# Kernel tuning notes

Measured on AMD Instinct MI355X. Metric: run time of the kernel, lower is better.

Reference implementation:

```python
import jax, jax.numpy as jnp
import numpy as np

HIDDEN = 1024
N_HEAD = 16
LN_EPS = 1e-5


def _layernorm(x, g, b):
    m = jnp.mean(x, axis=-1, keepdims=True)
    v = jnp.var(x, axis=-1, keepdims=True)
    return (x - m) * jax.lax.rsqrt(v + LN_EPS) * g + b


def setup_inputs() -> dict:
    key = jax.random.key(0)
    ks = jax.random.split(key, 16)
    H = HIDDEN
    s = 0.02
    d = dict(
        x=jax.random.normal(ks[0], (4, 1024, H), jnp.float32),
        Wq=jax.random.normal(ks[1], (H, H), jnp.float32) * s,
        bq=jnp.zeros((H,), jnp.float32),
        Wk=jax.random.normal(ks[2], (H, H), jnp.float32) * s,
        bk=jnp.zeros((H,), jnp.float32),
        Wv=jax.random.normal(ks[3], (H, H), jnp.float32) * s,
        bv=jnp.zeros((H,), jnp.float32),
        Wo=jax.random.normal(ks[4], (H, H), jnp.float32) * s,
        bo=jnp.zeros((H,), jnp.float32),
        g1=jax.random.normal(ks[5], (H,), jnp.float32) * s,
        b1=jnp.zeros((H,), jnp.float32),
        W1=jax.random.normal(ks[6], (H, 4 * H), jnp.float32) * s,
        c1=jnp.zeros((4 * H,), jnp.float32),
        W2=jax.random.normal(ks[7], (4 * H, H), jnp.float32) * s,
        c2=jnp.zeros((H,), jnp.float32),
        g2=jax.random.normal(ks[8], (H,), jnp.float32) * s,
        b2=jnp.zeros((H,), jnp.float32),
    )
    return d


def reference(x, Wq, bq, Wk, bk, Wv, bv, Wo, bo, g1, b1, W1, c1, W2, c2, g2, b2):
    N, T, Hd = x.shape
    Hh = N_HEAD
    D = Hd // Hh
    # faithful to torch code: .view(N, H, T, D) is a raw reshape, no transpose
    q = (x @ Wq + bq).reshape(N, Hh, T, D)
    k = (x @ Wk + bk).reshape(N, Hh, T, D)
    v = (x @ Wv + bv).reshape(N, Hh, T, D)
    scores = jnp.einsum('nhtd,nhsd->nhts', q, k) / jnp.sqrt(jnp.float32(Hd))
    # faithful: softmax over dim=1 (the head axis)
    attn = jax.nn.softmax(scores, axis=1)
    o = jnp.einsum('nhts,nhsd->nhtd', attn, v).reshape(N, T, Hd)
    o = o @ Wo + bo
    x1 = _layernorm(o + x, g1, b1)
    ff = jax.nn.gelu(x1 @ W1 + c1, approximate=False) @ W2 + c2
    return _layernorm(ff + x1, g2, b2)
```

## Files before the change

### kernel.cpp

```cpp
#include <hip/hip_runtime.h>
#include <cstdint>
#include <cstddef>

#define EPI_QKV  0
#define EPI_F32  2
#define EPI_GELU 3
#define EPI_PART 4

typedef __attribute__((ext_vector_type(8))) short bfrag8;
typedef __attribute__((ext_vector_type(4))) float facc4;

struct PtrQuad { unsigned short* p[4]; };

__device__ __forceinline__ unsigned short f2b(float x) {
  unsigned int u = __builtin_bit_cast(unsigned int, x);
  u += 0x7FFFu + ((u >> 16) & 1u);
  return (unsigned short)(u >> 16);
}
__device__ __forceinline__ float b2f(unsigned short u) {
  unsigned int x = ((unsigned int)u) << 16;
  return __builtin_bit_cast(float, x);
}

__device__ __forceinline__ void gl2lds16(const unsigned short* g, unsigned short* l) {
  __builtin_amdgcn_global_load_lds(
      (const __attribute__((address_space(1))) unsigned int*)g,
      (__attribute__((address_space(3))) unsigned int*)l, 16, 0, 0);
}

__global__ __launch_bounds__(256)
void cvt_bf16_kernel(const float* __restrict__ in, unsigned short* __restrict__ out, int n4) {
  const int i = blockIdx.x * 256 + threadIdx.x;
  if (i < n4) {
    const float4 v = ((const float4*)in)[i];
    ushort4 u;
    u.x = f2b(v.x); u.y = f2b(v.y); u.z = f2b(v.z); u.w = f2b(v.w);
    ((ushort4*)out)[i] = u;
  }
}

__global__ __launch_bounds__(256)
void transpose_cvt(const float* __restrict__ in, unsigned short* __restrict__ out,
                   int K, int N) {
  __shared__ float tile[32][33];
  const int n0 = blockIdx.x * 32;
  const int k0 = blockIdx.y * 32;
  const int tx = threadIdx.x & 31, ty = threadIdx.x >> 5;
#pragma unroll
  for (int i = 0; i < 32; i += 8)
    tile[ty + i][tx] = in[(size_t)(k0 + ty + i) * N + n0 + tx];
  __syncthreads();
#pragma unroll
  for (int i = 0; i < 32; i += 8)
    out[(size_t)(n0 + ty + i) * K + k0 + tx] = f2b(tile[tx][ty + i]);
}

template<int EPI>
__global__ __launch_bounds__(256, 2)
void gemm_bt(const unsigned short* __restrict__ A,
             const unsigned short* __restrict__ Bt,
             const float* __restrict__ bias,
             const float* __restrict__ bias2,
             const float* __restrict__ bias3,
             void* __restrict__ out, PtrQuad pq,
             int M, int N, int K, int ldk) {
  __shared__ unsigned short sA[128 * 32];
  __shared__ unsigned short sB[128 * 32];
  const int tid  = threadIdx.x;
  const int lane = tid & 63;
  const int wave = tid >> 6;
  const int l15  = lane & 15, l4 = lane >> 4;
  const int wr = wave >> 1, wc = wave & 1;
  const long row0 = (long)blockIdx.y * 128;
  const long col0 = (long)blockIdx.x * 128;
  const long k0   = (long)blockIdx.z * K;

  facc4 acc[4][4];
#pragma unroll
  for (int i = 0; i < 4; i++)
#pragma unroll
    for (int j = 0; j < 4; j++) acc[i][j] = (facc4)0.f;

  const int srow = tid >> 2;
  const int scol = (tid & 3) * 8;
  const unsigned short* Ap0 = A  + (row0 + srow) * (long)ldk + k0 + scol;
  const unsigned short* Ap1 = Ap0 + 64 * (long)ldk;
  const unsigned short* Bp0 = Bt + (col0 + srow) * (long)ldk + k0 + scol;
  const unsigned short* Bp1 = Bp0 + 64 * (long)ldk;
  const int wbase = (tid & ~63) * 8;
  unsigned short* sA0 = &sA[wbase];
  unsigned short* sA1 = &sA[2048 + wbase];
  unsigned short* sB0 = &sB[wbase];
  unsigned short* sB1 = &sB[2048 + wbase];

  const int aoff = (wr * 64 + l15) * 32 + l4 * 8;
  const int boff = (wc * 64 + l15) * 32 + l4 * 8;

  for (int kt = 0; kt < K; kt += 32) {
    gl2lds16(Ap0 + kt, sA0);
    gl2lds16(Ap1 + kt, sA1);
    gl2lds16(Bp0 + kt, sB0);
    gl2lds16(Bp1 + kt, sB1);
    __syncthreads();
    bfrag8 af[4], bf[4];
#pragma unroll
    for (int i = 0; i < 4; i++) af[i] = *(const bfrag8*)&sA[aoff + i * 512];
#pragma unroll
    for (int j = 0; j < 4; j++) bf[j] = *(const bfrag8*)&sB[boff + j * 512];
#pragma unroll
    for (int i = 0; i < 4; i++)
#pragma unroll
      for (int j = 0; j < 4; j++)
        acc[i][j] = __builtin_amdgcn_mfma_f32_16x16x32_bf16(af[i], bf[j], acc[i][j], 0, 0, 0);
    __syncthreads();
  }

#pragma unroll
  for (int i = 0; i < 4; i++) {
    const long m0 = row0 + wr * 64 + i * 16 + l4 * 4;
#pragma unroll
    for (int j = 0; j < 4; j++) {
      const long c = col0 + wc * 64 + j * 16 + l15;
      if constexpr (EPI == EPI_QKV) {
        const long which = c >> 10;
        const long cl = c & 1023;
        unsigned short* oq = (unsigned short*)out;
        if (which == 0) {
          const float bj = bias[cl];
#pragma unroll
          for (int r = 0; r < 4; r++)
            oq[(m0 + r) * 1024 + cl] = f2b((acc[i][j][r] + bj) * 0.03125f);
        } else if (which == 1) {
          const float bj = bias2[cl];
#pragma unroll
          for (int r = 0; r < 4; r++)
            (oq + 4194304)[(m0 + r) * 1024 + cl] = f2b(acc[i][j][r] + bj);
        } else {
          const float bj = bias3[cl];
          const long cc = cl >> 6, d = cl & 63;
#pragma unroll
          for (int r = 0; r < 4; r++) {
            const long m = m0 + r;
            const long nbb = m >> 10, rr = m & 1023;
            const long h = rr >> 6, rhi = rr & 63;
            const long s = rhi * 16 + cc;
            (oq + 8388608)[((nbb * 16 + h) * 64 + d) * 1024 + s] = f2b(acc[i][j][r] + bj);
          }
        }
      } else if constexpr (EPI == EPI_F32) {
        const float bj = bias[c];
        float* of = (float*)out;
#pragma unroll
        for (int r = 0; r < 4; r++) of[(m0 + r) * (long)N + c] = acc[i][j][r] + bj;
      } else if constexpr (EPI == EPI_PART) {
        unsigned short* ob = pq.p[blockIdx.z];
#pragma unroll
        for (int r = 0; r < 4; r++) ob[(m0 + r) * (long)N + c] = f2b(acc[i][j][r]);
      } else {
        const float bj = bias[c];
        unsigned short* ob = (unsigned short*)out;
#pragma unroll
        for (int r = 0; r < 4; r++) {
          const float t = acc[i][j][r] + bj;
          ob[(m0 + r) * (long)N + c] = f2b(0.5f * t * (1.f + erff(t * 0.70710678f)));
        }
      }
    }
  }
}

__global__ __launch_bounds__(512, 4)
void attn_kernel(const unsigned short* __restrict__ Qb,
                 const unsigned short* __restrict__ Kb,
                 const unsigned short* __restrict__ Vt,
                 unsigned short* __restrict__ P0, unsigned short* __restrict__ P1) {
  const int id = blockIdx.x;
  const int combo = id & 7;
  const int tile = id >> 3;
  const int nb = combo & 3;
  const int sp = combo >> 2;
  const int tid = threadIdx.x, lane = tid & 63;
  const int w = __builtin_amdgcn_readfirstlane(tid >> 6);
  const int l15 = lane & 15, l4 = lane >> 4;
  const int t0 = tile * 16;

  __shared__ float red[2][8][576];
  __shared__ __align__(16) unsigned short abuf[8][16][40];

  const size_t hb0 = (size_t)(nb * 16 + w * 2) << 16;
  const unsigned short* qB = Qb + hb0;
  const unsigned short* kB = Kb + hb0;
  const unsigned short* vB = Vt + hb0;

  bfrag8 qf[2][2];
#pragma unroll
  for (int hh = 0; hh < 2; hh++)
#pragma unroll
    for (int ks = 0; ks < 2; ks++)
      qf[hh][ks] = *(const bfrag8*)(qB + (hh << 16) + (t0 + l15) * 64 + ks * 32 + l4 * 8);

  facc4 oacc[2][4];
#pragma unroll
  for (int hh = 0; hh < 2; hh++)
#pragma unroll
    for (int nt = 0; nt < 4; nt++) oacc[hh][nt] = (facc4)0.f;

  for (int it = 0; it < 16; ++it) {
    const int s0 = sp * 512 + it * 32;
    const int pb = it & 1;
    facc4 sacc[2][2];
#pragma unroll
    for (int hh = 0; hh < 2; hh++)
#pragma unroll
      for (int nt = 0; nt < 2; nt++) sacc[hh][nt] = (facc4)0.f;
#pragma unroll
    for (int hh = 0; hh < 2; hh++) {
      const unsigned short* kh = kB + (hh << 16);
#pragma unroll
      for (int ks = 0; ks < 2; ks++)
#pragma unroll
        for (int nt = 0; nt < 2; nt++) {
          const bfrag8 kf = *(const bfrag8*)(kh + (s0 + nt * 16 + l15) * 64 + ks * 32 + l4 * 8);
          sacc[hh][nt] = __builtin_amdgcn_mfma_f32_16x16x32_bf16(qf[hh][ks], kf, sacc[hh][nt], 0, 0, 0);
        }
    }
    bfrag8 vf0[4], vf1[4];
#pragma unroll
    for (int nt = 0; nt < 4; nt++) {
      vf0[nt] = *(const bfrag8*)(vB + (size_t)(nt * 16 + l15) * 1024 + s0 + l4 * 8);
      vf1[nt] = *(const bfrag8*)(vB + (1 << 16) + (size_t)(nt * 16 + l15) * 1024 + s0 + l4 * 8);
    }
#pragma unroll
    for (int nt = 0; nt < 2; nt++)
#pragma unroll
      for (int r = 0; r < 4; r++) {
        const float e0 = __expf(sacc[0][nt][r]);
        const float e1 = __expf(sacc[1][nt][r]);
        sacc[0][nt][r] = e0; sacc[1][nt][r] = e1;
        red[pb][w][(l4 * 4 + r) * 36 + nt * 16 + l15] = e0 + e1;
      }
    __syncthreads();
    float rinv[2][4];
#pragma unroll
    for (int nt = 0; nt < 2; nt++)
#pragma unroll
      for (int r = 0; r < 4; r++) {
        const int o = (l4 * 4 + r) * 36 + nt * 16 + l15;
        float s = 0.f;
#pragma unroll
        for (int ww = 0; ww < 8; ww++) s += red[pb][ww][o];
        rinv[nt][r] = 1.f / s;
      }
#pragma unroll
    for (int nt = 0; nt < 2; nt++)
#pragma unroll
      for (int r = 0; r < 4; r++)
        abuf[w][l4 * 4 + r][nt * 16 + l15] = f2b(sacc[0][nt][r] * rinv[nt][r]);
    {
      const bfrag8 af0 = *(const bfrag8*)&abuf[w][l15][l4 * 8];
#pragma unroll
      for (int nt = 0; nt < 4; nt++)
        oacc[0][nt] = __builtin_amdgcn_mfma_f32_16x16x32_bf16(af0, vf0[nt], oacc[0][nt], 0, 0, 0);
    }
#pragma unroll
    for (int nt = 0; nt < 2; nt++)
#pragma unroll
      for (int r = 0; r < 4; r++)
        abuf[w][l4 * 4 + r][nt * 16 + l15] = f2b(sacc[1][nt][r] * rinv[nt][r]);
    {
      const bfrag8 af1 = *(const bfrag8*)&abuf[w][l15][l4 * 8];
#pragma unroll
      for (int nt = 0; nt < 4; nt++)
        oacc[1][nt] = __builtin_amdgcn_mfma_f32_16x16x32_bf16(af1, vf1[nt], oacc[1][nt], 0, 0, 0);
    }
  }
  unsigned short* P = sp ? P1 : P0;
#pragma unroll
  for (int hh = 0; hh < 2; hh++) {
    const size_t rb = ((size_t)nb * 1024 + (size_t)(w * 2 + hh) * 64 + tile) * 1024;
#pragma unroll
    for (int nt = 0; nt < 4; nt++)
#pragma unroll
      for (int r = 0; r < 4; r++)
        P[rb + (size_t)(l4 * 4 + r) * 64 + nt * 16 + l15] = f2b(oacc[hh][nt][r]);
  }
}

__global__ __launch_bounds__(256)
void reduce_o2(const unsigned short* __restrict__ P0, const unsigned short* __restrict__ P1,
               unsigned short* __restrict__ OB, int n4) {
  const int i = blockIdx.x * 256 + threadIdx.x;
  if (i < n4) {
    const ushort4 a = ((const ushort4*)P0)[i];
    const ushort4 b = ((const ushort4*)P1)[i];
    ushort4 u;
    u.x = f2b(b2f(a.x) + b2f(b.x));
    u.y = f2b(b2f(a.y) + b2f(b.y));
    u.z = f2b(b2f(a.z) + b2f(b.z));
    u.w = f2b(b2f(a.w) + b2f(b.w));
    ((ushort4*)OB)[i] = u;
  }
}

__global__ __launch_bounds__(256)
void ln_red(const unsigned short* __restrict__ P0, const unsigned short* __restrict__ P1,
            const unsigned short* __restrict__ P2, const unsigned short* __restrict__ P3,
            const float* __restrict__ bias, const float* __restrict__ resid,
            const float* __restrict__ g, const float* __restrict__ be,
            float* __restrict__ outf, unsigned short* __restrict__ outb) {
  const int row = blockIdx.x, tid = threadIdx.x;
  const size_t o4 = (size_t)row * 256 + tid;
  const ushort4 a = ((const ushort4*)P0)[o4];
  const ushort4 b = ((const ushort4*)P1)[o4];
  const ushort4 c = ((const ushort4*)P2)[o4];
  const ushort4 d = ((const ushort4*)P3)[o4];
  const float4 vb = ((const float4*)bias)[tid];
  const float4 vr = ((const float4*)resid)[o4];
  float t0 = b2f(a.x) + b2f(b.x) + b2f(c.x) + b2f(d.x) + vb.x + vr.x;
  float t1 = b2f(a.y) + b2f(b.y) + b2f(c.y) + b2f(d.y) + vb.y + vr.y;
  float t2 = b2f(a.z) + b2f(b.z) + b2f(c.z) + b2f(d.z) + vb.z + vr.z;
  float t3 = b2f(a.w) + b2f(b.w) + b2f(c.w) + b2f(d.w) + vb.w + vr.w;
  float s = t0 + t1 + t2 + t3;
  float q = t0 * t0 + t1 * t1 + t2 * t2 + t3 * t3;
#pragma unroll
  for (int off = 32; off > 0; off >>= 1) {
    s += __shfl_down(s, off, 64);
    q += __shfl_down(q, off, 64);
  }
  __shared__ float rs_[4], rq_[4];
  if ((tid & 63) == 0) { rs_[tid >> 6] = s; rq_[tid >> 6] = q; }
  __syncthreads();
  const float S = rs_[0] + rs_[1] + rs_[2] + rs_[3];
  const float Q = rq_[0] + rq_[1] + rq_[2] + rq_[3];
  const float mean = S * (1.f / 1024.f);
  const float var  = Q * (1.f / 1024.f) - mean * mean;
  const float rstd = rsqrtf(var + 1e-5f);
  const float4 vg  = ((const float4*)g)[tid];
  const float4 vbe = ((const float4*)be)[tid];
  float o0 = (t0 - mean) * rstd * vg.x + vbe.x;
  float o1 = (t1 - mean) * rstd * vg.y + vbe.y;
  float o2 = (t2 - mean) * rstd * vg.z + vbe.z;
  float o3 = (t3 - mean) * rstd * vg.w + vbe.w;
  ((float4*)(outf + (size_t)row * 1024))[tid] = make_float4(o0, o1, o2, o3);
  if (outb != nullptr) {
    ushort4 u;
    u.x = f2b(o0); u.y = f2b(o1); u.z = f2b(o2); u.w = f2b(o3);
    ((ushort4*)(outb + (size_t)row * 1024))[tid] = u;
  }
}

extern "C" void kernel_launch(void* const* d_in, const int* in_sizes, int n_in,
                              void* d_out, int out_size, void* d_ws, size_t ws_size,
                              hipStream_t stream) {
  const float* x  = (const float*)d_in[0];
  const float* Wq = (const float*)d_in[1];
  const float* bq = (const float*)d_in[2];
  const float* Wk = (const float*)d_in[3];
  const float* bk = (const float*)d_in[4];
  const float* Wv = (const float*)d_in[5];
  const float* bv = (const float*)d_in[6];
  const float* Wo = (const float*)d_in[7];
  const float* bo = (const float*)d_in[8];
  const float* g1 = (const float*)d_in[9];
  const float* b1 = (const float*)d_in[10];
  const float* W1 = (const float*)d_in[11];
  const float* c1 = (const float*)d_in[12];
  const float* W2 = (const float*)d_in[13];
  const float* c2 = (const float*)d_in[14];
  const float* g2 = (const float*)d_in[15];
  const float* b2 = (const float*)d_in[16];
  float* out = (float*)d_out;

  char* ws = (char*)d_ws;
  unsigned short* XB  = (unsigned short*)(ws);
  unsigned short* WQT = (unsigned short*)(ws + 8388608);
  unsigned short* WKT = (unsigned short*)(ws + 10485760);
  unsigned short* WVT = (unsigned short*)(ws + 12582912);
  unsigned short* WOT = (unsigned short*)(ws + 14680064);
  unsigned short* W1T = (unsigned short*)(ws + 16777216);
  unsigned short* W2T = (unsigned short*)(ws + 25165824);
  float*          X1  = (float*)(ws + 33554432);
  unsigned short* X1B = (unsigned short*)(ws + 50331648);
  char* RB = ws + 58720256;
  unsigned short* QB  = (unsigned short*)(RB);
  unsigned short* KB  = (unsigned short*)(RB + 8388608);
  unsigned short* VT  = (unsigned short*)(RB + 16777216);
  unsigned short* OB  = (unsigned short*)(RB + 25165824);
  unsigned short* H1B = (unsigned short*)(RB);
  unsigned short* AP0 = (unsigned short*)(RB + 33554432);
  unsigned short* AP1 = (unsigned short*)(RB + 41943040);
  PtrQuad OPQ = { { QB, KB, VT, XB } };
  PtrQuad FPQ = { { XB, X1B, (unsigned short*)(RB + 33554432),
                    (unsigned short*)(RB + 41943040) } };
  PtrQuad ZQ = { { nullptr, nullptr, nullptr, nullptr } };

  const dim3 tb(256);
  cvt_bf16_kernel<<<dim3(4096), tb, 0, stream>>>(x, XB, 1048576);
  transpose_cvt<<<dim3(32, 32),  tb, 0, stream>>>(Wq, WQT, 1024, 1024);
  transpose_cvt<<<dim3(32, 32),  tb, 0, stream>>>(Wk, WKT, 1024, 1024);
  transpose_cvt<<<dim3(32, 32),  tb, 0, stream>>>(Wv, WVT, 1024, 1024);
  transpose_cvt<<<dim3(32, 32),  tb, 0, stream>>>(Wo, WOT, 1024, 1024);
  transpose_cvt<<<dim3(128, 32), tb, 0, stream>>>(W1, W1T, 1024, 4096);
  transpose_cvt<<<dim3(32, 128), tb, 0, stream>>>(W2, W2T, 4096, 1024);
  gemm_bt<EPI_QKV><<<dim3(24, 32), tb, 0, stream>>>(XB, WQT, bq, bk, bv, (void*)QB, ZQ,
                                                    4096, 3072, 1024, 1024);
  attn_kernel<<<dim3(512), dim3(512), 0, stream>>>(QB, KB, VT, AP0, AP1);
  reduce_o2<<<dim3(4096), tb, 0, stream>>>(AP0, AP1, OB, 1048576);
  gemm_bt<EPI_PART><<<dim3(8, 32, 4), tb, 0, stream>>>(OB, WOT, nullptr, nullptr, nullptr,
                                                       nullptr, OPQ, 4096, 1024, 256, 1024);
  ln_red<<<dim3(4096), tb, 0, stream>>>(QB, KB, VT, XB, bo, x, g1, b1, X1, X1B);
  gemm_bt<EPI_GELU><<<dim3(32, 32), tb, 0, stream>>>(X1B, W1T, c1, nullptr, nullptr,
                                                     (void*)H1B, ZQ, 4096, 4096, 1024, 1024);
  gemm_bt<EPI_PART><<<dim3(8, 32, 4), tb, 0, stream>>>(H1B, W2T, nullptr, nullptr, nullptr,
                                                       nullptr, FPQ, 4096, 1024, 1024, 4096);
  ln_red<<<dim3(4096), tb, 0, stream>>>(FPQ.p[0], FPQ.p[1], FPQ.p[2], FPQ.p[3], c2, X1,
                                        g2, b2, out, (unsigned short*)nullptr);
}
```

Baseline: 466.4 us.

## Use LDS atomics for cross-wave softmax sums and batch weight transposes

The attention kernel stops writing per-wave partial sums to LDS and having every thread sum eight slots. Each wave now atomically adds into one shared 3-way rotating buffer, and wave 0 clears the buffer due for reuse two iterations later. This cuts LDS footprint and read traffic but adds LDS float atomic contention, and the sum order becomes nondeterministic. Separately, the four 1024x1024 weight transposes are merged into a single launch using gridDim.z to reduce launch overhead.

```diff
diff --git a/kernel.cpp b/kernel.cpp
--- a/kernel.cpp
+++ b/kernel.cpp
@@ -53,6 +53,27 @@
 #pragma unroll
   for (int i = 0; i < 32; i += 8)
     out[(size_t)(n0 + ty + i) * K + k0 + tx] = f2b(tile[tx][ty + i]);
+}
+
+__global__ __launch_bounds__(256)
+void transpose_cvt4(const float* __restrict__ i0, const float* __restrict__ i1,
+                    const float* __restrict__ i2, const float* __restrict__ i3,
+                    unsigned short* __restrict__ o0, unsigned short* __restrict__ o1,
+                    unsigned short* __restrict__ o2, unsigned short* __restrict__ o3) {
+  const int z = blockIdx.z;
+  const float* in = (z == 0) ? i0 : (z == 1) ? i1 : (z == 2) ? i2 : i3;
+  unsigned short* out = (z == 0) ? o0 : (z == 1) ? o1 : (z == 2) ? o2 : o3;
+  __shared__ float tile[32][33];
+  const int n0 = blockIdx.x * 32;
+  const int k0 = blockIdx.y * 32;
+  const int tx = threadIdx.x & 31, ty = threadIdx.x >> 5;
+#pragma unroll
+  for (int i = 0; i < 32; i += 8)
+    tile[ty + i][tx] = in[(size_t)(k0 + ty + i) * 1024 + n0 + tx];
+  __syncthreads();
+#pragma unroll
+  for (int i = 0; i < 32; i += 8)
+    out[(size_t)(n0 + ty + i) * 1024 + k0 + tx] = f2b(tile[tx][ty + i]);
 }
 
 template<int EPI>
@@ -184,8 +205,10 @@
   const int l15 = lane & 15, l4 = lane >> 4;
   const int t0 = tile * 16;
 
-  __shared__ float red[2][8][576];
+  __shared__ float red[3][576];
   __shared__ __align__(16) unsigned short abuf[8][16][40];
+
+  for (int z = tid; z < 3 * 576; z += 512) (&red[0][0])[z] = 0.f;
 
   const size_t hb0 = (size_t)(nb * 16 + w * 2) << 16;
   const unsigned short* qB = Qb + hb0;
@@ -205,9 +228,11 @@
 #pragma unroll
     for (int nt = 0; nt < 4; nt++) oacc[hh][nt] = (facc4)0.f;
 
+  __syncthreads();
+
+  int b = 0;
   for (int it = 0; it < 16; ++it) {
     const int s0 = sp * 512 + it * 32;
-    const int pb = it & 1;
     facc4 sacc[2][2];
 #pragma unroll
     for (int hh = 0; hh < 2; hh++)
@@ -237,19 +262,18 @@
         const float e0 = __expf(sacc[0][nt][r]);
         const float e1 = __expf(sacc[1][nt][r]);
         sacc[0][nt][r] = e0; sacc[1][nt][r] = e1;
-        red[pb][w][(l4 * 4 + r) * 36 + nt * 16 + l15] = e0 + e1;
+        atomicAdd(&red[b][(l4 * 4 + r) * 36 + nt * 16 + l15], e0 + e1);
       }
     __syncthreads();
+    const int bz = (b == 0) ? 2 : b - 1;
     float rinv[2][4];
 #pragma unroll
     for (int nt = 0; nt < 2; nt++)
 #pragma unroll
       for (int r = 0; r < 4; r++) {
         const int o = (l4 * 4 + r) * 36 + nt * 16 + l15;
-        float s = 0.f;
-#pragma unroll
-        for (int ww = 0; ww < 8; ww++) s += red[pb][ww][o];
-        rinv[nt][r] = 1.f / s;
+        rinv[nt][r] = 1.f / red[b][o];
+        if (w == 0) red[bz][o] = 0.f;
       }
 #pragma unroll
     for (int nt = 0; nt < 2; nt++)
@@ -273,6 +297,7 @@
       for (int nt = 0; nt < 4; nt++)
         oacc[1][nt] = __builtin_amdgcn_mfma_f32_16x16x32_bf16(af1, vf1[nt], oacc[1][nt], 0, 0, 0);
     }
+    b = (b == 2) ? 0 : b + 1;
   }
   unsigned short* P = sp ? P1 : P0;
 #pragma unroll
@@ -396,10 +421,7 @@
 
   const dim3 tb(256);
   cvt_bf16_kernel<<<dim3(4096), tb, 0, stream>>>(x, XB, 1048576);
-  transpose_cvt<<<dim3(32, 32),  tb, 0, stream>>>(Wq, WQT, 1024, 1024);
-  transpose_cvt<<<dim3(32, 32),  tb, 0, stream>>>(Wk, WKT, 1024, 1024);
-  transpose_cvt<<<dim3(32, 32),  tb, 0, stream>>>(Wv, WVT, 1024, 1024);
-  transpose_cvt<<<dim3(32, 32),  tb, 0, stream>>>(Wo, WOT, 1024, 1024);
+  transpose_cvt4<<<dim3(32, 32, 4), tb, 0, stream>>>(Wq, Wk, Wv, Wo, WQT, WKT, WVT, WOT);
   transpose_cvt<<<dim3(128, 32), tb, 0, stream>>>(W1, W1T, 1024, 4096);
   transpose_cvt<<<dim3(32, 128), tb, 0, stream>>>(W2, W2T, 4096, 1024);
   gemm_bt<EPI_QKV><<<dim3(24, 32), tb, 0, stream>>>(XB, WQT, bq, bk, bv, (void*)QB, ZQ,
```

Measured after the change: 555.0 us. 1.19x slower.
